# Kernel tuning notes

Hardware: AMD Instinct MI355X
Metric: run time of the kernel (lower is better)

The kernel has to match this reference:

```python
import jax, jax.numpy as jnp
import numpy as np

X_SIZE = 512
G_SIZE = 512
OUT_SIZE = 512  # must equal h_size (= x_size) for the LSTM cell update
BATCH = 64
SEQ = 256


def setup_inputs() -> dict:
    key = jax.random.key(0)
    k1, k2, k3, k4 = jax.random.split(key, 4)
    x = jax.random.normal(k1, (BATCH, SEQ, X_SIZE), dtype=jnp.float32)
    g = jax.random.normal(k2, (BATCH, G_SIZE), dtype=jnp.float32)
    in_dim = X_SIZE + X_SIZE + G_SIZE  # [x; h; g]
    scale = 1.0 / np.sqrt(in_dim)
    W = jax.random.normal(k3, (in_dim, 4 * OUT_SIZE), dtype=jnp.float32) * scale
    b = jnp.zeros((4 * OUT_SIZE,), dtype=jnp.float32)
    return {"x": x, "g": g, "W": W, "b": b}


def _run_direction(x_tbd, g, W, b):
    # x_tbd: [T, B, x_size]; g: [B, g_size]
    B = x_tbd.shape[1]
    h0 = jnp.zeros((B, OUT_SIZE), dtype=x_tbd.dtype)
    c0 = jnp.zeros((B, OUT_SIZE), dtype=x_tbd.dtype)

    def step(carry, x_t):
        h, c = carry
        z = jnp.concatenate([x_t, h, g], axis=-1) @ W + b  # [B, 4*out]
        i, f, o, u = jnp.split(z, 4, axis=-1)
        c = jax.nn.sigmoid(f) * c + jax.nn.sigmoid(i) * jnp.tanh(u)
        h = jax.nn.sigmoid(o) * jnp.tanh(c)
        return (h, c), h  # cell output == hidden state

    (h, c), outs = jax.lax.scan(step, (h0, c0), x_tbd)
    return outs, h, c  # outs: [T, B, out]


def reference(x, g, W, b):
    # x: [B, T, x_size]
    x_tbd = jnp.swapaxes(x, 0, 1)  # [T, B, D]
    # forward direction
    o_fwd, h_f, c_f = _run_direction(x_tbd, g, W, b)
    # backward direction (original uses the SAME self.Cell weights for both)
    o_bwd, h_b, c_b = _run_direction(x_tbd[::-1], g, W, b)
    o_bwd = o_bwd[::-1]  # re-reverse to align time
    out = jnp.concatenate([o_fwd, o_bwd], axis=-1)  # [T, B, 2*out]
    out = jnp.swapaxes(out, 0, 1)  # [B, T, 2*out]
    h_state = jnp.concatenate([h_f, h_b], axis=-1)
    c_state = jnp.concatenate([c_f, c_b], axis=-1)
    return (out, h_state, c_state)
```

## Files before the change

### kernel.cpp

```cpp
#include <hip/hip_runtime.h>
#include <cstdint>
#include <cstddef>

#define SEQL   256
#define NBATCH 64
#define HDIM   512
#define ZDIM   2048
#define KDIM   1536

typedef __attribute__((ext_vector_type(8))) short short8;
typedef __attribute__((ext_vector_type(4))) float f32x4;
typedef __attribute__((ext_vector_type(2))) float f32x2;
typedef __attribute__((ext_vector_type(4))) float f4v;

static __device__ __forceinline__ unsigned short f2bf(float f) {
  union { float f; unsigned u; } v; v.f = f;
  unsigned u = v.u;
  unsigned r = (u + 0x7FFFu + ((u >> 16) & 1u)) >> 16;
  return (unsigned short)r;
}
static __device__ __forceinline__ float bf2f(unsigned short s) {
  union { unsigned u; float f; } v; v.u = ((unsigned)s) << 16; return v.f;
}
static __device__ __forceinline__ float sigm(float x)  { return 1.f / (1.f + __expf(-x)); }
static __device__ __forceinline__ float tanh_f(float x){ return 1.f - 2.f / (__expf(2.f * x) + 1.f); }

static __device__ __forceinline__ void gl_lds16(const void* g, void* l) {
  __builtin_amdgcn_global_load_lds((const __attribute__((address_space(1))) unsigned int*)g,
                                   (__attribute__((address_space(3))) unsigned int*)l, 16, 0, 0);
}


__global__ __launch_bounds__(256) void k_convx(const float* __restrict__ x,
                                               unsigned short* __restrict__ Xb) {
  int i = blockIdx.x * 256 + threadIdx.x;
  int k8 = (i & 63) * 8;
  int r  = i >> 6;
  int b  = r & 63, t = r >> 6;
  const float* src = x + ((size_t)(b * SEQL + t) * HDIM + k8);
  f4v v0 = *(const f4v*)src;
  f4v v1 = *(const f4v*)(src + 4);
  short8 o;
#pragma unroll
  for (int j = 0; j < 4; ++j) o[j] = (short)f2bf(v0[j]);
#pragma unroll
  for (int j = 0; j < 4; ++j) o[4 + j] = (short)f2bf(v1[j]);
  *(short8*)(Xb + (size_t)r * HDIM + k8) = o;
}

__global__ __launch_bounds__(256) void k_convg(const float* __restrict__ g,
                                               unsigned short* __restrict__ gbf) {
  int i = blockIdx.x * 256 + threadIdx.x;
  int k8 = (i & 63) * 8;
  int row = i >> 6;
  const float* src = g + ((size_t)row * HDIM + k8);
  f4v v0 = *(const f4v*)src;
  f4v v1 = *(const f4v*)(src + 4);
  short8 o;
#pragma unroll
  for (int j = 0; j < 4; ++j) o[j] = (short)f2bf(v0[j]);
#pragma unroll
  for (int j = 0; j < 4; ++j) o[4 + j] = (short)f2bf(v1[j]);
  *(short8*)(gbf + (size_t)row * HDIM + k8) = o;
}

__global__ __launch_bounds__(256) void k_trans(const float* __restrict__ W,
                                               unsigned short* __restrict__ Wt) {
  __shared__ float tile[32][33];
  int tx = threadIdx.x & 31, ty = threadIdx.x >> 5;
  int n0 = blockIdx.x * 32;
  int j0 = blockIdx.y * 32;
#pragma unroll
  for (int jj = 0; jj < 4; ++jj)
    tile[ty + jj * 8][tx] = W[(size_t)(j0 + ty + jj * 8) * ZDIM + n0 + tx];
  __syncthreads();
#pragma unroll
  for (int jj = 0; jj < 4; ++jj)
    Wt[(size_t)(n0 + ty + jj * 8) * KDIM + j0 + tx] = f2bf(tile[tx][ty + jj * 8]);
}

__global__ __launch_bounds__(256) void k_gb(const unsigned short* __restrict__ gbf,
                                            const unsigned short* __restrict__ Wt,
                                            const float* __restrict__ bias,
                                            float* __restrict__ gbuf) {
  int tid = threadIdx.x, l = tid & 63, w = tid >> 6;
  int n0 = blockIdx.x * 64 + w * 16;
  f32x4 acc[4] = {};
#pragma unroll
  for (int kb = 0; kb < 16; ++kb) {
    short8 bfr = *(const short8*)((const char*)Wt + (size_t)(n0 + (l & 15)) * 3072
                                  + 2048 + kb * 64 + (l >> 4) * 16);
#pragma unroll
    for (int mi = 0; mi < 4; ++mi) {
      short8 afr = *(const short8*)((const char*)gbf + (size_t)(mi * 16 + (l & 15)) * 1024
                                    + kb * 64 + (l >> 4) * 16);
      acc[mi] = __builtin_amdgcn_mfma_f32_16x16x32_bf16(afr, bfr, acc[mi], 0, 0, 0);
    }
  }
  int r0 = (l >> 4) * 4, cq = l & 15;
#pragma unroll
  for (int mi = 0; mi < 4; ++mi)
#pragma unroll
    for (int reg = 0; reg < 4; ++reg) {
      int row = mi * 16 + r0 + reg, col = n0 + cq;
      gbuf[(size_t)row * ZDIM + col] = acc[mi][reg] + bias[col];
    }
}

__global__ __launch_bounds__(256, 2) void k_gemm_p1(const unsigned short* __restrict__ Xb,
                                                    const unsigned short* __restrict__ Wt,
                                                    const float* __restrict__ gbuf,
                                                    unsigned short* __restrict__ zpre) {
  __shared__ unsigned char sm[32768];
  int tm = blockIdx.x, tn = blockIdx.y;
  int tid = threadIdx.x, l = tid & 63, w = tid >> 6;
  int m0w = (w & 1) * 64, n0w = (w >> 1) * 64;
  f32x4 acc[4][4] = {};

  for (int k0 = 0; k0 < HDIM; k0 += 64) {
#pragma unroll
    for (int j = 0; j < 8; ++j) {
      int c = j * 4 + w;
      int lane_row = l >> 3;
      int kb = (l & 7) * 16;
      const char* gsrc;
      if (c < 16) {
        int row = c * 8 + lane_row;
        gsrc = (const char*)Xb + (size_t)(tm * 128 + row) * 1024 + k0 * 2 + kb;
      } else {
        int row = (c - 16) * 8 + lane_row;
        gsrc = (const char*)Wt + (size_t)(tn * 128 + row) * 3072 + k0 * 2 + kb;
      }
      gl_lds16(gsrc, (char*)sm + c * 1024);
    }
    __syncthreads();

#pragma unroll
    for (int kk = 0; kk < 64; kk += 32) {
      short8 af[4], bf[4];
#pragma unroll
      for (int mi = 0; mi < 4; ++mi)
        af[mi] = *(const short8*)((const char*)sm + (size_t)(m0w + mi * 16 + (l & 15)) * 128
                                  + (kk + (l >> 4) * 8) * 2);
#pragma unroll
      for (int ni = 0; ni < 4; ++ni)
        bf[ni] = *(const short8*)((const char*)sm + 16384 + (size_t)(n0w + ni * 16 + (l & 15)) * 128
                                  + (kk + (l >> 4) * 8) * 2);
#pragma unroll
      for (int mi = 0; mi < 4; ++mi)
#pragma unroll
        for (int ni = 0; ni < 4; ++ni)
          acc[mi][ni] = __builtin_amdgcn_mfma_f32_16x16x32_bf16(af[mi], bf[ni], acc[mi][ni], 0, 0, 0);
    }
    __syncthreads();
  }

  int r0 = (l >> 4) * 4, cq = l & 15;
#pragma unroll
  for (int mi = 0; mi < 4; ++mi)
#pragma unroll
    for (int ni = 0; ni < 4; ++ni) {
      int col = tn * 128 + n0w + ni * 16 + cq;
#pragma unroll
      for (int reg = 0; reg < 4; ++reg) {
        int row = tm * 128 + m0w + mi * 16 + r0 + reg;
        float v = acc[mi][ni][reg] + gbuf[(size_t)(row & 63) * ZDIM + col];
        zpre[(size_t)row * ZDIM + col] = f2bf(v);
      }
    }
}


__global__ __launch_bounds__(256, 1) void k_rec(const unsigned short* __restrict__ Wt,
                                                const unsigned short* __restrict__ zpre,
                                                unsigned long long* __restrict__ hbuf8,
                                                float* __restrict__ out,
                                                float* __restrict__ hstate,
                                                float* __restrict__ cstate) {
  __shared__ short lwh[4 * 32 * 512];
  __shared__ unsigned char As[16 * 1024];
  __shared__ float zbuf[4][16][33];

  const int tid = threadIdx.x, l = tid & 63, gi = tid >> 6;
  const int bid = blockIdx.x;
  const int cg = bid & 15, gid = bid >> 4, dir = gid >> 2, bg = gid & 3;
  const int hc0 = cg * 32;

#pragma unroll
  for (int col = 0; col < 32; ++col) {
    int kbs = l * 16;
    int kbyte = kbs ^ ((col & 7) << 4);
    short8 v = *(const short8*)((const char*)Wt
                + (size_t)(gi * 512 + hc0 + col) * 3072 + 1024 + kbyte);
    *(short8*)((char*)lwh + gi * 32768 + col * 1024 + kbs) = v;
  }

  const int r = tid >> 4, q = tid & 15;
  float c0 = 0.f, c1 = 0.f, h0 = 0.f, h1 = 0.f;

  int t = dir ? (SEQL - 1) : 0;
  unsigned zp[4];
  {
    const char* zb = (const char*)zpre
        + (((size_t)t * 64 + bg * 16 + r) * ZDIM + hc0 + 2 * q) * 2;
#pragma unroll
    for (int gg = 0; gg < 4; ++gg) zp[gg] = *(const unsigned*)(zb + gg * 1024);
  }

  const size_t p_idx = ((size_t)(dir * 64 + bg * 16 + r)) * 256 + cg * 16 + q;
  const int c_row = l >> 4, c_cp = l & 15;

  for (int s = 0; s < SEQL; ++s) {
    f32x4 acc0 = {0.f, 0.f, 0.f, 0.f}, acc1 = {0.f, 0.f, 0.f, 0.f};

    if (s) {
      const unsigned expect = (unsigned)(s - 1);
      const unsigned long long* hb = hbuf8 + (size_t)((s - 1) & 1) * 32768;
      unsigned long long v[16];
      int gd = 0;
      bool ok;
      do {
#pragma unroll
        for (int it = 0; it < 4; ++it)
#pragma unroll
          for (int kk = 0; kk < 4; ++kk) {
            int row = it * 4 + c_row;
            int kb = gi * 4 + kk;
            v[it * 4 + kk] = __hip_atomic_load(
                hb + ((size_t)(dir * 64 + bg * 16 + row)) * 256 + kb * 16 + c_cp,
                __ATOMIC_RELAXED, __HIP_MEMORY_SCOPE_SYSTEM);
          }
        ok = true;
#pragma unroll
        for (int i = 0; i < 16; ++i) ok = ok && ((unsigned)(v[i] >> 32) == expect);
      } while (!__all(ok) && ++gd < (1 << 16));

#pragma unroll
      for (int it = 0; it < 4; ++it)
#pragma unroll
        for (int kk = 0; kk < 4; ++kk) {
          int row = it * 4 + c_row;
          int kb = gi * 4 + kk;
          int byte = (row * 1024 + kb * 64 + c_cp * 4) ^ ((row & 7) << 4);
          *(unsigned*)(As + byte) = (unsigned)v[it * 4 + kk];
        }
    }
    __syncthreads();

    if (s) {
#pragma unroll
      for (int kb = 0; kb < 16; ++kb) {
        int arow = l & 15;
        int abyte = (arow * 1024 + kb * 64 + (l >> 4) * 16) ^ ((arow & 7) << 4);
        short8 a = *(const short8*)(As + abyte);
        int kfrag = kb * 64 + (l >> 4) * 16;
        int kbyte = kfrag ^ ((l & 7) << 4);
        short8 b0 = *(const short8*)((const char*)lwh + gi * 32768 + (size_t)(l & 15) * 1024 + kbyte);
        short8 b1 = *(const short8*)((const char*)lwh + gi * 32768 + (size_t)(16 + (l & 15)) * 1024 + kbyte);
        acc0 = __builtin_amdgcn_mfma_f32_16x16x32_bf16(a, b0, acc0, 0, 0, 0);
        acc1 = __builtin_amdgcn_mfma_f32_16x16x32_bf16(a, b1, acc1, 0, 0, 0);
      }
    }

    {
      int col = l & 15, row0 = (l >> 4) * 4;
#pragma unroll
      for (int reg = 0; reg < 4; ++reg) {
        zbuf[gi][row0 + reg][col]      = acc0[reg];
        zbuf[gi][row0 + reg][col + 16] = acc1[reg];
      }
    }
    __syncthreads();

    float zi0 = zbuf[0][r][2 * q]     + bf2f((unsigned short)(zp[0] & 0xffffu));
    float zi1 = zbuf[0][r][2 * q + 1] + bf2f((unsigned short)(zp[0] >> 16));
    float zf0 = zbuf[1][r][2 * q]     + bf2f((unsigned short)(zp[1] & 0xffffu));
    float zf1 = zbuf[1][r][2 * q + 1] + bf2f((unsigned short)(zp[1] >> 16));
    float zo0 = zbuf[2][r][2 * q]     + bf2f((unsigned short)(zp[2] & 0xffffu));
    float zo1 = zbuf[2][r][2 * q + 1] + bf2f((unsigned short)(zp[2] >> 16));
    float zu0 = zbuf[3][r][2 * q]     + bf2f((unsigned short)(zp[3] & 0xffffu));
    float zu1 = zbuf[3][r][2 * q + 1] + bf2f((unsigned short)(zp[3] >> 16));

    c0 = sigm(zf0) * c0 + sigm(zi0) * tanh_f(zu0);
    h0 = sigm(zo0) * tanh_f(c0);
    c1 = sigm(zf1) * c1 + sigm(zi1) * tanh_f(zu1);
    h1 = sigm(zo1) * tanh_f(c1);

    {
      unsigned hd = (unsigned)f2bf(h0) | ((unsigned)f2bf(h1) << 16);
      unsigned long long pv = (unsigned long long)hd
                            | ((unsigned long long)(unsigned)s << 32);
      __hip_atomic_store(hbuf8 + (size_t)(s & 1) * 32768 + p_idx, pv,
                         __ATOMIC_RELAXED, __HIP_MEMORY_SCOPE_SYSTEM);
    }

    {
      f32x2 ho; ho.x = h0; ho.y = h1;
      __builtin_nontemporal_store(ho, reinterpret_cast<f32x2*>(
          out + ((size_t)(bg * 16 + r) * SEQL + t) * 1024 + dir * 512 + hc0 + 2 * q));
    }
    if (s + 1 < SEQL) {
      t = dir ? (SEQL - 2 - s) : (s + 1);
      const char* zb = (const char*)zpre
          + (((size_t)t * 64 + bg * 16 + r) * ZDIM + hc0 + 2 * q) * 2;
#pragma unroll
      for (int gg = 0; gg < 4; ++gg) zp[gg] = *(const unsigned*)(zb + gg * 1024);
    }
  }

  {
    size_t st = (size_t)(bg * 16 + r) * 1024 + dir * 512 + hc0 + 2 * q;
    f32x2 hv; hv.x = h0; hv.y = h1;
    f32x2 cv2; cv2.x = c0; cv2.y = c1;
    __builtin_nontemporal_store(hv, reinterpret_cast<f32x2*>(hstate + st));
    __builtin_nontemporal_store(cv2, reinterpret_cast<f32x2*>(cstate + st));
  }
}


extern "C" void kernel_launch(void* const* d_in, const int* in_sizes, int n_in,
                              void* d_out, int out_size, void* d_ws, size_t ws_size,
                              hipStream_t stream) {
  const float* x    = (const float*)d_in[0];
  const float* g    = (const float*)d_in[1];
  const float* W    = (const float*)d_in[2];
  const float* bias = (const float*)d_in[3];
  float* out = (float*)d_out;
  float* hstate = out + (size_t)16777216;
  float* cstate = out + (size_t)16842752;

  char* ws = (char*)d_ws;
  unsigned long long* hbuf8 = (unsigned long long*)(ws + 0);
  unsigned short* Xb   = (unsigned short*)(ws + 524288);
  unsigned short* Wt   = (unsigned short*)(ws + 17301504);
  unsigned short* gbf  = (unsigned short*)(ws + 23592960);
  float*          gbuf = (float*)(ws + 23658496);
  unsigned short* zpre = (unsigned short*)(ws + 24182784);

  hipMemsetAsync((void*)hbuf8, 0xFF, 524288, stream);

  k_convx<<<4096, 256, 0, stream>>>(x, Xb);
  k_convg<<<16, 256, 0, stream>>>(g, gbf);
  k_trans<<<dim3(64, 48), 256, 0, stream>>>(W, Wt);
  k_gb<<<32, 256, 0, stream>>>(gbf, Wt, bias, gbuf);
  k_gemm_p1<<<dim3(128, 16), 256, 0, stream>>>(Xb, Wt, gbuf, zpre);
  k_rec<<<128, 256, 0, stream>>>(Wt, zpre, hbuf8, out, hstate, cstate);
}
```

Baseline: 781.3 us.

## Vectorize recurrent h polling with dwordx4 loads and cache-scoped stores, remap blocks

```diff
diff --git a/kernel.cpp b/kernel.cpp
--- a/kernel.cpp
+++ b/kernel.cpp
@@ -12,6 +12,8 @@
 typedef __attribute__((ext_vector_type(4))) float f32x4;
 typedef __attribute__((ext_vector_type(2))) float f32x2;
 typedef __attribute__((ext_vector_type(4))) float f4v;
+typedef __attribute__((ext_vector_type(4))) unsigned uint4v;
+typedef unsigned long long ull;
 
 static __device__ __forceinline__ unsigned short f2bf(float f) {
   union { float f; unsigned u; } v; v.f = f;
@@ -173,7 +175,7 @@
 
 __global__ __launch_bounds__(256, 1) void k_rec(const unsigned short* __restrict__ Wt,
                                                 const unsigned short* __restrict__ zpre,
-                                                unsigned long long* __restrict__ hbuf8,
+                                                ull* __restrict__ hbuf8,
                                                 float* __restrict__ out,
                                                 float* __restrict__ hstate,
                                                 float* __restrict__ cstate) {
@@ -183,7 +185,8 @@
 
   const int tid = threadIdx.x, l = tid & 63, gi = tid >> 6;
   const int bid = blockIdx.x;
-  const int cg = bid & 15, gid = bid >> 4, dir = gid >> 2, bg = gid & 3;
+  const int gid = bid & 7, cg = bid >> 3;
+  const int dir = gid >> 2, bg = gid & 3;
   const int hc0 = cg * 32;
 
 #pragma unroll
@@ -208,42 +211,62 @@
   }
 
   const size_t p_idx = ((size_t)(dir * 64 + bg * 16 + r)) * 256 + cg * 16 + q;
-  const int c_row = l >> 4, c_cp = l & 15;
+  const int prow = l >> 3;
+  const int cp8 = (l & 7) * 8;
 
   for (int s = 0; s < SEQL; ++s) {
     f32x4 acc0 = {0.f, 0.f, 0.f, 0.f}, acc1 = {0.f, 0.f, 0.f, 0.f};
 
     if (s) {
-      const unsigned expect = (unsigned)(s - 1);
-      const unsigned long long* hb = hbuf8 + (size_t)((s - 1) & 1) * 32768;
-      unsigned long long v[16];
-      int gd = 0;
-      bool ok;
+      const unsigned e = (unsigned)(s - 1);
+      const char* rg = (const char*)hbuf8 + (size_t)((s - 1) & 1) * 262144;
+      const char* b0 = rg + (size_t)(dir * 64 + bg * 16 + prow) * 2048
+                          + gi * 512 + (l & 7) * 16;
+      const char* b1 = b0 + 16384;
+      uint4v A0, A1, B0, B1, C0, C1, D0, D1;
+      int gd = 0; bool ok;
+#define LQ2(OFF, SC, V0, V1) \
+      asm volatile("global_load_dwordx4 %0, %2, off offset:" OFF " " SC "\n\t" \
+                   "global_load_dwordx4 %1, %3, off offset:" OFF " " SC \
+                   : "=&v"(V0), "=&v"(V1) : "v"(b0), "v"(b1) : "memory")
       do {
-#pragma unroll
-        for (int it = 0; it < 4; ++it)
-#pragma unroll
-          for (int kk = 0; kk < 4; ++kk) {
-            int row = it * 4 + c_row;
-            int kb = gi * 4 + kk;
-            v[it * 4 + kk] = __hip_atomic_load(
-                hb + ((size_t)(dir * 64 + bg * 16 + row)) * 256 + kb * 16 + c_cp,
-                __ATOMIC_RELAXED, __HIP_MEMORY_SCOPE_SYSTEM);
-          }
-        ok = true;
-#pragma unroll
-        for (int i = 0; i < 16; ++i) ok = ok && ((unsigned)(v[i] >> 32) == expect);
-      } while (!__all(ok) && ++gd < (1 << 16));
-
-#pragma unroll
-      for (int it = 0; it < 4; ++it)
-#pragma unroll
-        for (int kk = 0; kk < 4; ++kk) {
-          int row = it * 4 + c_row;
-          int kb = gi * 4 + kk;
-          int byte = (row * 1024 + kb * 64 + c_cp * 4) ^ ((row & 7) << 4);
-          *(unsigned*)(As + byte) = (unsigned)v[it * 4 + kk];
+        if ((gd & 3) != 3) {
+          LQ2("0",   "sc0", A0, A1);
+          LQ2("128", "sc0", B0, B1);
+          LQ2("256", "sc0", C0, C1);
+          LQ2("384", "sc0", D0, D1);
+        } else {
+          LQ2("0",   "sc0 sc1", A0, A1);
+          LQ2("128", "sc0 sc1", B0, B1);
+          LQ2("256", "sc0 sc1", C0, C1);
+          LQ2("384", "sc0 sc1", D0, D1);
         }
+        asm volatile("s_waitcnt vmcnt(0)"
+          : "+v"(A0), "+v"(A1), "+v"(B0), "+v"(B1),
+            "+v"(C0), "+v"(C1), "+v"(D0), "+v"(D1) :: "memory");
+        __builtin_amdgcn_sched_barrier(0);
+        ok = (A0[1] == e) && (A0[3] == e) && (A1[1] == e) && (A1[3] == e)
+          && (B0[1] == e) && (B0[3] == e) && (B1[1] == e) && (B1[3] == e)
+          && (C0[1] == e) && (C0[3] == e) && (C1[1] == e) && (C1[3] == e)
+          && (D0[1] == e) && (D0[3] == e) && (D1[1] == e) && (D1[3] == e);
+      } while (!__all(ok) && ++gd < (1 << 18));
+#undef LQ2
+
+      {
+        const int r0b = prow * 1024 + gi * 256 + cp8;
+        const int r1b = (prow + 8) * 1024 + gi * 256 + cp8;
+        const int x = (prow & 7) << 4;
+#define PKD(V) ((ull)V[0] | ((ull)V[2] << 32))
+        *(ull*)(As + ((r0b +   0) ^ x)) = PKD(A0);
+        *(ull*)(As + ((r1b +   0) ^ x)) = PKD(A1);
+        *(ull*)(As + ((r0b +  64) ^ x)) = PKD(B0);
+        *(ull*)(As + ((r1b +  64) ^ x)) = PKD(B1);
+        *(ull*)(As + ((r0b + 128) ^ x)) = PKD(C0);
+        *(ull*)(As + ((r1b + 128) ^ x)) = PKD(C1);
+        *(ull*)(As + ((r0b + 192) ^ x)) = PKD(D0);
+        *(ull*)(As + ((r1b + 192) ^ x)) = PKD(D1);
+#undef PKD
+      }
     }
     __syncthreads();
 
@@ -255,10 +278,10 @@
         short8 a = *(const short8*)(As + abyte);
         int kfrag = kb * 64 + (l >> 4) * 16;
         int kbyte = kfrag ^ ((l & 7) << 4);
-        short8 b0 = *(const short8*)((const char*)lwh + gi * 32768 + (size_t)(l & 15) * 1024 + kbyte);
-        short8 b1 = *(const short8*)((const char*)lwh + gi * 32768 + (size_t)(16 + (l & 15)) * 1024 + kbyte);
-        acc0 = __builtin_amdgcn_mfma_f32_16x16x32_bf16(a, b0, acc0, 0, 0, 0);
-        acc1 = __builtin_amdgcn_mfma_f32_16x16x32_bf16(a, b1, acc1, 0, 0, 0);
+        short8 b0v = *(const short8*)((const char*)lwh + gi * 32768 + (size_t)(l & 15) * 1024 + kbyte);
+        short8 b1v = *(const short8*)((const char*)lwh + gi * 32768 + (size_t)(16 + (l & 15)) * 1024 + kbyte);
+        acc0 = __builtin_amdgcn_mfma_f32_16x16x32_bf16(a, b0v, acc0, 0, 0, 0);
+        acc1 = __builtin_amdgcn_mfma_f32_16x16x32_bf16(a, b1v, acc1, 0, 0, 0);
       }
     }
 
@@ -288,10 +311,10 @@
 
     {
       unsigned hd = (unsigned)f2bf(h0) | ((unsigned)f2bf(h1) << 16);
-      unsigned long long pv = (unsigned long long)hd
-                            | ((unsigned long long)(unsigned)s << 32);
-      __hip_atomic_store(hbuf8 + (size_t)(s & 1) * 32768 + p_idx, pv,
-                         __ATOMIC_RELAXED, __HIP_MEMORY_SCOPE_SYSTEM);
+      ull pv = (ull)hd | ((ull)(unsigned)s << 32);
+      ull* ps = hbuf8 + (size_t)(s & 1) * 32768 + p_idx;
+      asm volatile("global_store_dwordx2 %0, %1, off sc0 sc1" :: "v"(ps), "v"(pv) : "memory");
+      asm volatile("global_store_dwordx2 %0, %1, off sc0"     :: "v"(ps), "v"(pv) : "memory");
     }
 
     {
@@ -330,7 +353,7 @@
   float* cstate = out + (size_t)16842752;
 
   char* ws = (char*)d_ws;
-  unsigned long long* hbuf8 = (unsigned long long*)(ws + 0);
+  ull* hbuf8 = (ull*)(ws + 0);
   unsigned short* Xb   = (unsigned short*)(ws + 524288);
   unsigned short* Wt   = (unsigned short*)(ws + 17301504);
   unsigned short* gbf  = (unsigned short*)(ws + 23592960);
```

Result: slower. 946.4 us (+21.1%).

## Remap recurrent MFMA outputs to drop zbuf LDS exchange and second barrier

Applied to the files above, without the earlier changes.

```diff
diff --git a/kernel.cpp b/kernel.cpp
--- a/kernel.cpp
+++ b/kernel.cpp
@@ -12,6 +12,7 @@
 typedef __attribute__((ext_vector_type(4))) float f32x4;
 typedef __attribute__((ext_vector_type(2))) float f32x2;
 typedef __attribute__((ext_vector_type(4))) float f4v;
+typedef unsigned long long ull;
 
 static __device__ __forceinline__ unsigned short f2bf(float f) {
   union { float f; unsigned u; } v; v.f = f;
@@ -173,13 +174,12 @@
 
 __global__ __launch_bounds__(256, 1) void k_rec(const unsigned short* __restrict__ Wt,
                                                 const unsigned short* __restrict__ zpre,
-                                                unsigned long long* __restrict__ hbuf8,
+                                                ull* __restrict__ hbuf8,
                                                 float* __restrict__ out,
                                                 float* __restrict__ hstate,
                                                 float* __restrict__ cstate) {
   __shared__ short lwh[4 * 32 * 512];
   __shared__ unsigned char As[16 * 1024];
-  __shared__ float zbuf[4][16][33];
 
   const int tid = threadIdx.x, l = tid & 63, gi = tid >> 6;
   const int bid = blockIdx.x;
@@ -195,125 +195,126 @@
     *(short8*)((char*)lwh + gi * 32768 + col * 1024 + kbs) = v;
   }
 
-  const int r = tid >> 4, q = tid & 15;
-  float c0 = 0.f, c1 = 0.f, h0 = 0.f, h1 = 0.f;
-
-  int t = dir ? (SEQL - 1) : 0;
-  unsigned zp[4];
+  const bool hi8 = (l & 8) != 0;
+  const int r0  = (l >> 4) * 4 + (hi8 ? 2 : 0);
+  const int p   = r0 >> 1;
+  const int hcf = hc0 + gi * 8 + (l & 7);
+  float cs0 = 0.f, cs1 = 0.f, hh0 = 0.f, hh1 = 0.f;
+
+  unsigned short zp[8];
   {
-    const char* zb = (const char*)zpre
-        + (((size_t)t * 64 + bg * 16 + r) * ZDIM + hc0 + 2 * q) * 2;
-#pragma unroll
-    for (int gg = 0; gg < 4; ++gg) zp[gg] = *(const unsigned*)(zb + gg * 1024);
-  }
-
-  const size_t p_idx = ((size_t)(dir * 64 + bg * 16 + r)) * 256 + cg * 16 + q;
-  const int c_row = l >> 4, c_cp = l & 15;
+    int t0 = dir ? (SEQL - 1) : 0;
+    const unsigned short* zb = zpre + ((size_t)t0 * 64 + bg * 16 + r0) * ZDIM + hcf;
+#pragma unroll
+    for (int g = 0; g < 4; ++g) { zp[g * 2] = zb[g * 512]; zp[g * 2 + 1] = zb[2048 + g * 512]; }
+  }
+
+  const int rp = l >> 3;
+  const size_t pbase = ((size_t)(dir * 4 + bg) * 8 + rp) * 512 + (l & 7) * 4;
 
   for (int s = 0; s < SEQL; ++s) {
+    int t = dir ? (SEQL - 1 - s) : s;
     f32x4 acc0 = {0.f, 0.f, 0.f, 0.f}, acc1 = {0.f, 0.f, 0.f, 0.f};
 
     if (s) {
-      const unsigned expect = (unsigned)(s - 1);
-      const unsigned long long* hb = hbuf8 + (size_t)((s - 1) & 1) * 32768;
-      unsigned long long v[16];
-      int gd = 0;
-      bool ok;
+      const unsigned e = (unsigned)(s - 1);
+      const ull* hb = hbuf8 + (size_t)((s - 1) & 1) * 32768;
+      ull v[16];
+      int gd = 0; bool ok;
       do {
 #pragma unroll
-        for (int it = 0; it < 4; ++it)
-#pragma unroll
-          for (int kk = 0; kk < 4; ++kk) {
-            int row = it * 4 + c_row;
-            int kb = gi * 4 + kk;
-            v[it * 4 + kk] = __hip_atomic_load(
-                hb + ((size_t)(dir * 64 + bg * 16 + row)) * 256 + kb * 16 + c_cp,
-                __ATOMIC_RELAXED, __HIP_MEMORY_SCOPE_SYSTEM);
-          }
+        for (int kk = 0; kk < 4; ++kk)
+#pragma unroll
+          for (int j = 0; j < 4; ++j)
+            v[kk * 4 + j] = __hip_atomic_load(hb + pbase + (size_t)(gi * 4 + kk) * 32 + j,
+                                              __ATOMIC_RELAXED, __HIP_MEMORY_SCOPE_SYSTEM);
         ok = true;
 #pragma unroll
-        for (int i = 0; i < 16; ++i) ok = ok && ((unsigned)(v[i] >> 32) == expect);
-      } while (!__all(ok) && ++gd < (1 << 16));
-
-#pragma unroll
-      for (int it = 0; it < 4; ++it)
-#pragma unroll
-        for (int kk = 0; kk < 4; ++kk) {
-          int row = it * 4 + c_row;
-          int kb = gi * 4 + kk;
-          int byte = (row * 1024 + kb * 64 + c_cp * 4) ^ ((row & 7) << 4);
-          *(unsigned*)(As + byte) = (unsigned)v[it * 4 + kk];
-        }
+        for (int i = 0; i < 16; ++i) ok = ok && ((unsigned)(v[i] >> 32) == e);
+      } while (!__all(ok) && ++gd < (1 << 17));
+
+#pragma unroll
+      for (int kk = 0; kk < 4; ++kk) {
+        int kb = gi * 4 + kk;
+        unsigned d0 = (unsigned)v[kk * 4 + 0], d1 = (unsigned)v[kk * 4 + 1];
+        unsigned d2 = (unsigned)v[kk * 4 + 2], d3 = (unsigned)v[kk * 4 + 3];
+        unsigned lo0 = __builtin_amdgcn_perm(d1, d0, 0x05040100u);
+        unsigned lo1 = __builtin_amdgcn_perm(d3, d2, 0x05040100u);
+        unsigned hi0 = __builtin_amdgcn_perm(d1, d0, 0x07060302u);
+        unsigned hi1 = __builtin_amdgcn_perm(d3, d2, 0x07060302u);
+        int row0 = rp * 2, row1 = row0 + 1;
+        int cb = kb * 64 + (l & 7) * 8;
+        *(ull*)(As + ((row0 * 1024 + cb) ^ ((row0 & 7) << 4))) = (ull)lo0 | ((ull)lo1 << 32);
+        *(ull*)(As + ((row1 * 1024 + cb) ^ ((row1 & 7) << 4))) = (ull)hi0 | ((ull)hi1 << 32);
+      }
     }
     __syncthreads();
 
     if (s) {
+      const int gsel = (l >> 3) & 1;
+      const int colb = (gi * 8 + (l & 7)) * 1024;
 #pragma unroll
       for (int kb = 0; kb < 16; ++kb) {
         int arow = l & 15;
         int abyte = (arow * 1024 + kb * 64 + (l >> 4) * 16) ^ ((arow & 7) << 4);
         short8 a = *(const short8*)(As + abyte);
-        int kfrag = kb * 64 + (l >> 4) * 16;
-        int kbyte = kfrag ^ ((l & 7) << 4);
-        short8 b0 = *(const short8*)((const char*)lwh + gi * 32768 + (size_t)(l & 15) * 1024 + kbyte);
-        short8 b1 = *(const short8*)((const char*)lwh + gi * 32768 + (size_t)(16 + (l & 15)) * 1024 + kbyte);
+        int kbyte = (kb * 64 + (l >> 4) * 16) ^ ((l & 7) << 4);
+        short8 b0 = *(const short8*)((const char*)lwh + gsel * 32768 + colb + kbyte);
+        short8 b1 = *(const short8*)((const char*)lwh + (2 + gsel) * 32768 + colb + kbyte);
         acc0 = __builtin_amdgcn_mfma_f32_16x16x32_bf16(a, b0, acc0, 0, 0, 0);
         acc1 = __builtin_amdgcn_mfma_f32_16x16x32_bf16(a, b1, acc1, 0, 0, 0);
       }
     }
 
+    float sa0[4], sa1[4];
+#pragma unroll
+    for (int k2 = 0; k2 < 4; ++k2) {
+      sa0[k2] = __shfl_xor(acc0[k2], 8, 64);
+      sa1[k2] = __shfl_xor(acc1[k2], 8, 64);
+    }
     {
-      int col = l & 15, row0 = (l >> 4) * 4;
-#pragma unroll
-      for (int reg = 0; reg < 4; ++reg) {
-        zbuf[gi][row0 + reg][col]      = acc0[reg];
-        zbuf[gi][row0 + reg][col + 16] = acc1[reg];
-      }
-    }
-    __syncthreads();
-
-    float zi0 = zbuf[0][r][2 * q]     + bf2f((unsigned short)(zp[0] & 0xffffu));
-    float zi1 = zbuf[0][r][2 * q + 1] + bf2f((unsigned short)(zp[0] >> 16));
-    float zf0 = zbuf[1][r][2 * q]     + bf2f((unsigned short)(zp[1] & 0xffffu));
-    float zf1 = zbuf[1][r][2 * q + 1] + bf2f((unsigned short)(zp[1] >> 16));
-    float zo0 = zbuf[2][r][2 * q]     + bf2f((unsigned short)(zp[2] & 0xffffu));
-    float zo1 = zbuf[2][r][2 * q + 1] + bf2f((unsigned short)(zp[2] >> 16));
-    float zu0 = zbuf[3][r][2 * q]     + bf2f((unsigned short)(zp[3] & 0xffffu));
-    float zu1 = zbuf[3][r][2 * q + 1] + bf2f((unsigned short)(zp[3] >> 16));
-
-    c0 = sigm(zf0) * c0 + sigm(zi0) * tanh_f(zu0);
-    h0 = sigm(zo0) * tanh_f(c0);
-    c1 = sigm(zf1) * c1 + sigm(zi1) * tanh_f(zu1);
-    h1 = sigm(zo1) * tanh_f(c1);
-
+      float zi_ = (hi8 ? sa0[2] : acc0[0]) + bf2f(zp[0]);
+      float zf_ = (hi8 ? acc0[2] : sa0[0]) + bf2f(zp[2]);
+      float zo_ = (hi8 ? sa1[2] : acc1[0]) + bf2f(zp[4]);
+      float zu_ = (hi8 ? acc1[2] : sa1[0]) + bf2f(zp[6]);
+      cs0 = sigm(zf_) * cs0 + sigm(zi_) * tanh_f(zu_);
+      hh0 = sigm(zo_) * tanh_f(cs0);
+    }
     {
-      unsigned hd = (unsigned)f2bf(h0) | ((unsigned)f2bf(h1) << 16);
-      unsigned long long pv = (unsigned long long)hd
-                            | ((unsigned long long)(unsigned)s << 32);
+      float zi_ = (hi8 ? sa0[3] : acc0[1]) + bf2f(zp[1]);
+      float zf_ = (hi8 ? acc0[3] : sa0[1]) + bf2f(zp[3]);
+      float zo_ = (hi8 ? sa1[3] : acc1[1]) + bf2f(zp[5]);
+      float zu_ = (hi8 ? acc1[3] : sa1[1]) + bf2f(zp[7]);
+      cs1 = sigm(zf_) * cs1 + sigm(zi_) * tanh_f(zu_);
+      hh1 = sigm(zo_) * tanh_f(cs1);
+    }
+
+    {
+      unsigned hd = (unsigned)f2bf(hh0) | ((unsigned)f2bf(hh1) << 16);
+      ull pv = (ull)hd | ((ull)(unsigned)s << 32);
+      size_t p_idx = ((size_t)(dir * 4 + bg) * 8 + p) * 512 + hcf;
       __hip_atomic_store(hbuf8 + (size_t)(s & 1) * 32768 + p_idx, pv,
                          __ATOMIC_RELAXED, __HIP_MEMORY_SCOPE_SYSTEM);
     }
 
-    {
-      f32x2 ho; ho.x = h0; ho.y = h1;
-      __builtin_nontemporal_store(ho, reinterpret_cast<f32x2*>(
-          out + ((size_t)(bg * 16 + r) * SEQL + t) * 1024 + dir * 512 + hc0 + 2 * q));
-    }
+    __builtin_nontemporal_store(hh0,
+        out + ((size_t)(bg * 16 + r0) * SEQL + t) * 1024 + dir * 512 + hcf);
+    __builtin_nontemporal_store(hh1,
+        out + ((size_t)(bg * 16 + r0 + 1) * SEQL + t) * 1024 + dir * 512 + hcf);
     if (s + 1 < SEQL) {
-      t = dir ? (SEQL - 2 - s) : (s + 1);
-      const char* zb = (const char*)zpre
-          + (((size_t)t * 64 + bg * 16 + r) * ZDIM + hc0 + 2 * q) * 2;
-#pragma unroll
-      for (int gg = 0; gg < 4; ++gg) zp[gg] = *(const unsigned*)(zb + gg * 1024);
+      int tn = dir ? (SEQL - 2 - s) : (s + 1);
+      const unsigned short* zb = zpre + ((size_t)tn * 64 + bg * 16 + r0) * ZDIM + hcf;
+#pragma unroll
+      for (int g = 0; g < 4; ++g) { zp[g * 2] = zb[g * 512]; zp[g * 2 + 1] = zb[2048 + g * 512]; }
     }
   }
 
   {
-    size_t st = (size_t)(bg * 16 + r) * 1024 + dir * 512 + hc0 + 2 * q;
-    f32x2 hv; hv.x = h0; hv.y = h1;
-    f32x2 cv2; cv2.x = c0; cv2.y = c1;
-    __builtin_nontemporal_store(hv, reinterpret_cast<f32x2*>(hstate + st));
-    __builtin_nontemporal_store(cv2, reinterpret_cast<f32x2*>(cstate + st));
+    size_t st = (size_t)(bg * 16 + r0) * 1024 + dir * 512 + hcf;
+    __builtin_nontemporal_store(hh0, hstate + st);
+    __builtin_nontemporal_store(cs0, cstate + st);
+    __builtin_nontemporal_store(hh1, hstate + st + 1024);
+    __builtin_nontemporal_store(cs1, cstate + st + 1024);
   }
 }
 
@@ -330,7 +331,7 @@
   float* cstate = out + (size_t)16842752;
 
   char* ws = (char*)d_ws;
-  unsigned long long* hbuf8 = (unsigned long long*)(ws + 0);
+  ull* hbuf8 = (ull*)(ws + 0);
   unsigned short* Xb   = (unsigned short*)(ws + 524288);
   unsigned short* Wt   = (unsigned short*)(ws + 17301504);
   unsigned short* gbf  = (unsigned short*)(ws + 23592960);
```

After: 884.9 us. 13.3% more time.
